# Kernel tuning notes

Measured on AMD Instinct MI355X. Metric: run time of the kernel, lower is better.

The kernel has to match this reference:

```python
import jax, jax.numpy as jnp
import numpy as np

INPUT_SIZE = 2
EMB = 64
RNN = 128
EDGE_RNN = 128
OUT = 5
N = 500000


def setup_inputs() -> dict:
    key = jax.random.key(0)
    ks = jax.random.split(key, 12)
    s = 0.1
    return {
        "pos": jax.random.normal(ks[0], (N, INPUT_SIZE), jnp.float32),
        "h_other": jax.random.normal(ks[1], (N, 2 * EDGE_RNN), jnp.float32),
        "h": jax.random.normal(ks[2], (N, RNN), jnp.float32),
        "enc_W": jax.random.normal(ks[3], (EMB, INPUT_SIZE), jnp.float32) * s,
        "enc_b": jnp.zeros((EMB,), jnp.float32),
        "henc_W": jax.random.normal(ks[4], (EMB, 2 * EDGE_RNN), jnp.float32) * s,
        "henc_b": jnp.zeros((EMB,), jnp.float32),
        "W_ih": jax.random.normal(ks[5], (3 * RNN, 2 * EMB), jnp.float32) * s,
        "b_ih": jax.random.normal(ks[6], (3 * RNN,), jnp.float32) * s,
        "W_hh": jax.random.normal(ks[7], (3 * RNN, RNN), jnp.float32) * s,
        "b_hh": jax.random.normal(ks[8], (3 * RNN,), jnp.float32) * s,
        "dec_W": jax.random.normal(ks[9], (OUT, RNN), jnp.float32) * s,
        "dec_b": jnp.zeros((OUT,), jnp.float32),
    }


def reference(pos, h_other, h, enc_W, enc_b, henc_W, henc_b,
              W_ih, b_ih, W_hh, b_hh, dec_W, dec_b):
    # encode position and edge-RNN hidden states
    enc_in = jax.nn.relu(pos @ enc_W.T + enc_b)          # [N, EMB]
    enc_hid = jax.nn.relu(h_other @ henc_W.T + henc_b)   # [N, EMB]
    x = jnp.concatenate([enc_in, enc_hid], axis=1)       # [N, 2*EMB]
    # GRUCell (torch gate order: reset, update, new)
    gx = x @ W_ih.T + b_ih                               # [N, 3*RNN]
    gh = h @ W_hh.T + b_hh                               # [N, 3*RNN]
    xr, xz, xn = jnp.split(gx, 3, axis=1)
    hr, hz, hn = jnp.split(gh, 3, axis=1)
    r = jax.nn.sigmoid(xr + hr)
    z = jax.nn.sigmoid(xz + hz)
    n = jnp.tanh(xn + r * hn)
    h_new = (1.0 - z) * n + z * h                        # [N, RNN]
    out = h_new @ dec_W.T + dec_b                        # [N, OUT]
    return (out, h_new)
```

## Files before the change

kernel.cpp:

```cpp
#include <hip/hip_runtime.h>
#include <hip/hip_bf16.h>
#include <stdint.h>

typedef __bf16 bf16x8 __attribute__((ext_vector_type(8)));
typedef float f32x4 __attribute__((ext_vector_type(4)));

#define WS_WIH 0
#define WS_WHH 49152
#define WS_HENC 98304
#define WS_DEC 114688
#define WS_TOTAL 116736

#define LDS_X  0
#define LDS_H  16384
#define LDS_SZ 32768

__device__ __forceinline__ unsigned short f2bf(float f) {
    unsigned u = __float_as_uint(f);
    unsigned r = (u + 0x7FFFu + ((u >> 16) & 1u)) >> 16;
    return (unsigned short)r;
}
__device__ __forceinline__ float bf2f(unsigned short u) {
    return __uint_as_float(((unsigned)u) << 16);
}

__device__ __forceinline__ unsigned cvt_pk_bf16(float a, float b) {
    unsigned r;
    asm("v_cvt_pk_bf16_f32 %0, %1, %2" : "=v"(r) : "v"(a), "v"(b));
    return r;
}

__device__ __forceinline__ float fast_rcp(float x) { return __builtin_amdgcn_rcpf(x); }
__device__ __forceinline__ float sigmf(float x) { return fast_rcp(1.0f + __expf(-x)); }
__device__ __forceinline__ float tanh_fast(float x) {
    float t = __expf(-2.0f * fabsf(x));
    float r = (1.0f - t) * fast_rcp(1.0f + t);
    return copysignf(r, x);
}

__global__ void convert_weights_kernel(const float* __restrict__ wih,
                                       const float* __restrict__ whh,
                                       const float* __restrict__ henc,
                                       const float* __restrict__ dec,
                                       unsigned short* __restrict__ ws) {
    int i = blockIdx.x * 256 + threadIdx.x;
    if (i >= WS_TOTAL) return;
    float v;
    if (i < WS_WHH)        v = wih[i];
    else if (i < WS_HENC)  v = whh[i - WS_WHH];
    else if (i < WS_DEC)   v = henc[i - WS_HENC];
    else { int d = i - WS_DEC; v = (d < 640) ? dec[d] : 0.0f; }
    ws[i] = f2bf(v);
}

__launch_bounds__(256, 2)
__global__ void fused_rnn_kernel(const float* __restrict__ pos,
                                 const float* __restrict__ h_other,
                                 const float* __restrict__ h,
                                 const float* __restrict__ enc_W,
                                 const float* __restrict__ enc_b,
                                 const float* __restrict__ henc_b,
                                 const float* __restrict__ b_ih,
                                 const float* __restrict__ b_hh,
                                 const float* __restrict__ dec_b,
                                 const unsigned short* __restrict__ ws,
                                 float* __restrict__ out,
                                 float* __restrict__ hnew,
                                 int N) {
    __shared__ char sm[LDS_SZ];
    const int tid = threadIdx.x;
    const int w   = tid >> 6;
    const int l   = tid & 63;
    const int lg  = l >> 4;
    const int ln  = l & 15;
    const int row0 = blockIdx.x * 64;

    #pragma unroll
    for (int j = 0; j < 8; ++j) {
        int e0  = (tid + 256 * j) * 4;
        int row = e0 >> 7;
        int col = e0 & 127;
        int grow = row0 + row; if (grow > N - 1) grow = N - 1;
        float4 v = *reinterpret_cast<const float4*>(h + (size_t)grow * 128 + col);
        uint2 p;
        p.x = cvt_pk_bf16(v.x, v.y);
        p.y = cvt_pk_bf16(v.z, v.w);
        int boff = LDS_H + row * 256 + ((col * 2) ^ ((row & 7) << 4));
        *reinterpret_cast<uint2*>(sm + boff) = p;
    }
    {
        int row = tid >> 2;
        int c0  = (tid & 3) * 16;
        int grow = row0 + row; if (grow > N - 1) grow = N - 1;
        float p0 = pos[(size_t)grow * 2 + 0];
        float p1 = pos[(size_t)grow * 2 + 1];
        #pragma unroll
        for (int q = 0; q < 8; ++q) {
            int c = c0 + q * 2;
            float v0 = fmaxf(p0 * enc_W[c * 2]     + p1 * enc_W[c * 2 + 1] + enc_b[c], 0.f);
            float v1 = fmaxf(p0 * enc_W[c * 2 + 2] + p1 * enc_W[c * 2 + 3] + enc_b[c + 1], 0.f);
            unsigned pk = cvt_pk_bf16(v0, v1);
            int boff = LDS_X + row * 256 + ((c * 2) ^ ((row & 7) << 4));
            *reinterpret_cast<unsigned*>(sm + boff) = pk;
        }
    }

    {
        bf16x8 Bh[8];
        const unsigned short* hb = ws + WS_HENC + (size_t)(16 * w + ln) * 256;
        #pragma unroll
        for (int ks = 0; ks < 8; ++ks)
            Bh[ks] = *reinterpret_cast<const bf16x8*>(hb + ks * 32 + lg * 8);

        f32x4 e2[4];
        #pragma unroll
        for (int mt = 0; mt < 4; ++mt) e2[mt] = (f32x4){0.f, 0.f, 0.f, 0.f};
        #pragma unroll
        for (int mt = 0; mt < 4; ++mt) {
            int grow = row0 + 16 * mt + ln; if (grow > N - 1) grow = N - 1;
            const float* rp = h_other + (size_t)grow * 256 + lg * 8;
            #pragma unroll
            for (int ks = 0; ks < 8; ++ks) {
                const float* ap = rp + ks * 32;
                float4 a0 = *reinterpret_cast<const float4*>(ap);
                float4 a1 = *reinterpret_cast<const float4*>(ap + 4);
                union { unsigned u[4]; bf16x8 b; } af;
                af.u[0] = cvt_pk_bf16(a0.x, a0.y);
                af.u[1] = cvt_pk_bf16(a0.z, a0.w);
                af.u[2] = cvt_pk_bf16(a1.x, a1.y);
                af.u[3] = cvt_pk_bf16(a1.z, a1.w);
                e2[mt] = __builtin_amdgcn_mfma_f32_16x16x32_bf16(af.b, Bh[ks], e2[mt], 0, 0, 0);
            }
        }
        int col = 16 * w + ln;
        float bias = henc_b[col];
        #pragma unroll
        for (int mt = 0; mt < 4; ++mt)
            #pragma unroll
            for (int i = 0; i < 4; ++i) {
                int row = 16 * mt + lg * 4 + i;
                float v = fmaxf(e2[mt][i] + bias, 0.f);
                *reinterpret_cast<unsigned short*>(
                    sm + LDS_X + row * 256 + (((64 + col) * 2) ^ ((row & 7) << 4))) = f2bf(v);
            }
    }
    __syncthreads();

    f32x4 acc[4][8];
    #pragma unroll
    for (int a = 0; a < 4; ++a)
        #pragma unroll
        for (int b = 0; b < 8; ++b) acc[a][b] = (f32x4){0.f, 0.f, 0.f, 0.f};

    const unsigned short* WIH = ws + WS_WIH;
    const unsigned short* WHH = ws + WS_WHH;

    #pragma unroll
    for (int t = 0; t < 8; ++t) {
        const int abase = (t < 4) ? LDS_X : LDS_H;
        const int kb = (t & 3) * 64;
        bf16x8 Af[4];
        #pragma unroll
        for (int mt = 0; mt < 4; ++mt) {
            int row = 16 * mt + ln;
            Af[mt] = *reinterpret_cast<const bf16x8*>(
                sm + abase + row * 256 + ((kb + lg * 16) ^ ((row & 7) << 4)));
        }
        const int kk = (t & 3) * 32 + lg * 8;

        #define MFMA_JOB(job, Wptr, ob) { \
            bf16x8 bfr = *reinterpret_cast<const bf16x8*>((Wptr) + (size_t)((ob) + ln) * 128 + kk); \
            acc[0][job] = __builtin_amdgcn_mfma_f32_16x16x32_bf16(Af[0], bfr, acc[0][job], 0, 0, 0); \
            acc[1][job] = __builtin_amdgcn_mfma_f32_16x16x32_bf16(Af[1], bfr, acc[1][job], 0, 0, 0); \
            acc[2][job] = __builtin_amdgcn_mfma_f32_16x16x32_bf16(Af[2], bfr, acc[2][job], 0, 0, 0); \
            acc[3][job] = __builtin_amdgcn_mfma_f32_16x16x32_bf16(Af[3], bfr, acc[3][job], 0, 0, 0); }

        if (t < 4) {
            MFMA_JOB(0, WIH, 32 * w);
            MFMA_JOB(1, WIH, 32 * w + 16);
            MFMA_JOB(2, WIH, 128 + 32 * w);
            MFMA_JOB(3, WIH, 144 + 32 * w);
            MFMA_JOB(4, WIH, 256 + 32 * w);
            MFMA_JOB(5, WIH, 272 + 32 * w);
        } else {
            MFMA_JOB(0, WHH, 32 * w);
            MFMA_JOB(1, WHH, 32 * w + 16);
            MFMA_JOB(2, WHH, 128 + 32 * w);
            MFMA_JOB(3, WHH, 144 + 32 * w);
            MFMA_JOB(6, WHH, 256 + 32 * w);
            MFMA_JOB(7, WHH, 272 + 32 * w);
        }
        #undef MFMA_JOB
    }

    __syncthreads();

    #pragma unroll
    for (int jt = 0; jt < 2; ++jt) {
        int j = 32 * w + 16 * jt + ln;
        float br  = b_ih[j] + b_hh[j];
        float bz  = b_ih[128 + j] + b_hh[128 + j];
        float bxn = b_ih[256 + j];
        float bhn = b_hh[256 + j];
        #pragma unroll
        for (int mt = 0; mt < 4; ++mt)
            #pragma unroll
            for (int i = 0; i < 4; ++i) {
                int row = mt * 16 + lg * 4 + i;
                int grow = row0 + row;
                float r  = sigmf(acc[mt][jt][i] + br);
                float z  = sigmf(acc[mt][2 + jt][i] + bz);
                float xn = acc[mt][4 + jt][i] + bxn;
                float hn = acc[mt][6 + jt][i] + bhn;
                float nn = tanh_fast(xn + r * hn);
                unsigned short hu = *reinterpret_cast<const unsigned short*>(
                    sm + LDS_H + row * 256 + ((j * 2) ^ ((row & 7) << 4)));
                float hp = bf2f(hu);
                float hv = (1.0f - z) * nn + z * hp;
                if (grow < N) hnew[(size_t)grow * 128 + j] = hv;
                *reinterpret_cast<unsigned short*>(
                    sm + LDS_X + row * 256 + ((j * 2) ^ ((row & 7) << 4))) = f2bf(hv);
            }
    }
    __syncthreads();

    {
        f32x4 oc = (f32x4){0.f, 0.f, 0.f, 0.f};
        #pragma unroll
        for (int ks = 0; ks < 4; ++ks) {
            int row = 16 * w + ln;
            bf16x8 af = *reinterpret_cast<const bf16x8*>(
                sm + LDS_X + row * 256 + ((ks * 64 + lg * 16) ^ ((row & 7) << 4)));
            bf16x8 bf = *reinterpret_cast<const bf16x8*>(ws + WS_DEC + ln * 128 + ks * 32 + lg * 8);
            oc = __builtin_amdgcn_mfma_f32_16x16x32_bf16(af, bf, oc, 0, 0, 0);
        }
        if (ln < 5) {
            float bias = dec_b[ln];
            #pragma unroll
            for (int i = 0; i < 4; ++i) {
                int grow = row0 + 16 * w + lg * 4 + i;
                if (grow < N) out[(size_t)grow * 5 + ln] = oc[i] + bias;
            }
        }
    }
}

extern "C" void kernel_launch(void* const* d_in, const int* in_sizes, int n_in,
                              void* d_out, int out_size, void* d_ws, size_t ws_size,
                              hipStream_t stream) {
    const float* pos     = (const float*)d_in[0];
    const float* h_other = (const float*)d_in[1];
    const float* h       = (const float*)d_in[2];
    const float* enc_W   = (const float*)d_in[3];
    const float* enc_b   = (const float*)d_in[4];
    const float* henc_W  = (const float*)d_in[5];
    const float* henc_b  = (const float*)d_in[6];
    const float* W_ih    = (const float*)d_in[7];
    const float* b_ih    = (const float*)d_in[8];
    const float* W_hh    = (const float*)d_in[9];
    const float* b_hh    = (const float*)d_in[10];
    const float* dec_W   = (const float*)d_in[11];
    const float* dec_b   = (const float*)d_in[12];

    int N = in_sizes[0] / 2;
    unsigned short* ws = (unsigned short*)d_ws;
    float* out  = (float*)d_out;
    float* hnew = out + (size_t)N * 5;

    hipLaunchKernelGGL(convert_weights_kernel, dim3((WS_TOTAL + 255) / 256), dim3(256), 0, stream,
                       W_ih, W_hh, henc_W, dec_W, ws);
    int blocks = (N + 63) / 64;
    hipLaunchKernelGGL(fused_rnn_kernel, dim3(blocks), dim3(256), 0, stream,
                       pos, h_other, h, enc_W, enc_b, henc_b, b_ih, b_hh, dec_b,
                       ws, out, hnew, N);
}
```

Baseline: 556.3 us.

## Use 512-thread blocks with per-wave gate columns and double-buffered weight fragments

Doubles the workgroup to 8 waves per 64-row tile, so each wave owns 16 hidden columns and computes all three gates for them, with half the accumulators. Weight fragments are software-pipelined with ping-pong registers so the next k-step's global loads are issued before the current MFMAs. The h_other encoder loads are batched before conversion, and the henc and decoder weights are hoisted. The aim is more latency hiding and less register pressure per wave. In exchange each wave issues fewer MFMAs, and half the waves sit idle in the decoder stage.

```diff
diff --git a/kernel.cpp b/kernel.cpp
--- a/kernel.cpp
+++ b/kernel.cpp
@@ -53,7 +53,7 @@
     ws[i] = f2bf(v);
 }
 
-__launch_bounds__(256, 2)
+__launch_bounds__(512, 2)
 __global__ void fused_rnn_kernel(const float* __restrict__ pos,
                                  const float* __restrict__ h_other,
                                  const float* __restrict__ h,
@@ -75,9 +75,18 @@
     const int ln  = l & 15;
     const int row0 = blockIdx.x * 64;
 
+    const int nt = w & 3;
+    bf16x8 Bh[8];
+    {
+        const unsigned short* hb = ws + WS_HENC + (size_t)(16 * nt + ln) * 256;
+        #pragma unroll
+        for (int ks = 0; ks < 8; ++ks)
+            Bh[ks] = *reinterpret_cast<const bf16x8*>(hb + ks * 32 + lg * 8);
+    }
+
     #pragma unroll
-    for (int j = 0; j < 8; ++j) {
-        int e0  = (tid + 256 * j) * 4;
+    for (int j = 0; j < 4; ++j) {
+        int e0  = (tid + 512 * j) * 4;
         int row = e0 >> 7;
         int col = e0 & 127;
         int grow = row0 + row; if (grow > N - 1) grow = N - 1;
@@ -89,13 +98,13 @@
         *reinterpret_cast<uint2*>(sm + boff) = p;
     }
     {
-        int row = tid >> 2;
-        int c0  = (tid & 3) * 16;
+        int row = tid >> 3;
+        int c0  = (tid & 7) * 8;
         int grow = row0 + row; if (grow > N - 1) grow = N - 1;
         float p0 = pos[(size_t)grow * 2 + 0];
         float p1 = pos[(size_t)grow * 2 + 1];
         #pragma unroll
-        for (int q = 0; q < 8; ++q) {
+        for (int q = 0; q < 4; ++q) {
             int c = c0 + q * 2;
             float v0 = fmaxf(p0 * enc_W[c * 2]     + p1 * enc_W[c * 2 + 1] + enc_b[c], 0.f);
             float v1 = fmaxf(p0 * enc_W[c * 2 + 2] + p1 * enc_W[c * 2 + 3] + enc_b[c + 1], 0.f);
@@ -106,133 +115,138 @@
     }
 
     {
-        bf16x8 Bh[8];
-        const unsigned short* hb = ws + WS_HENC + (size_t)(16 * w + ln) * 256;
-        #pragma unroll
-        for (int ks = 0; ks < 8; ++ks)
-            Bh[ks] = *reinterpret_cast<const bf16x8*>(hb + ks * 32 + lg * 8);
-
-        f32x4 e2[4];
-        #pragma unroll
-        for (int mt = 0; mt < 4; ++mt) e2[mt] = (f32x4){0.f, 0.f, 0.f, 0.f};
-        #pragma unroll
-        for (int mt = 0; mt < 4; ++mt) {
+        f32x4 e2[2];
+        #pragma unroll
+        for (int m2 = 0; m2 < 2; ++m2) e2[m2] = (f32x4){0.f, 0.f, 0.f, 0.f};
+        #pragma unroll
+        for (int m2 = 0; m2 < 2; ++m2) {
+            int mt = (w >> 2) * 2 + m2;
             int grow = row0 + 16 * mt + ln; if (grow > N - 1) grow = N - 1;
             const float* rp = h_other + (size_t)grow * 256 + lg * 8;
+            float4 hb0[8], hb1[8];
             #pragma unroll
             for (int ks = 0; ks < 8; ++ks) {
-                const float* ap = rp + ks * 32;
-                float4 a0 = *reinterpret_cast<const float4*>(ap);
-                float4 a1 = *reinterpret_cast<const float4*>(ap + 4);
+                hb0[ks] = *reinterpret_cast<const float4*>(rp + ks * 32);
+                hb1[ks] = *reinterpret_cast<const float4*>(rp + ks * 32 + 4);
+            }
+            #pragma unroll
+            for (int ks = 0; ks < 8; ++ks) {
                 union { unsigned u[4]; bf16x8 b; } af;
-                af.u[0] = cvt_pk_bf16(a0.x, a0.y);
-                af.u[1] = cvt_pk_bf16(a0.z, a0.w);
-                af.u[2] = cvt_pk_bf16(a1.x, a1.y);
-                af.u[3] = cvt_pk_bf16(a1.z, a1.w);
-                e2[mt] = __builtin_amdgcn_mfma_f32_16x16x32_bf16(af.b, Bh[ks], e2[mt], 0, 0, 0);
-            }
-        }
-        int col = 16 * w + ln;
+                af.u[0] = cvt_pk_bf16(hb0[ks].x, hb0[ks].y);
+                af.u[1] = cvt_pk_bf16(hb0[ks].z, hb0[ks].w);
+                af.u[2] = cvt_pk_bf16(hb1[ks].x, hb1[ks].y);
+                af.u[3] = cvt_pk_bf16(hb1[ks].z, hb1[ks].w);
+                e2[m2] = __builtin_amdgcn_mfma_f32_16x16x32_bf16(af.b, Bh[ks], e2[m2], 0, 0, 0);
+            }
+        }
+        int col = 16 * nt + ln;
         float bias = henc_b[col];
         #pragma unroll
-        for (int mt = 0; mt < 4; ++mt)
+        for (int m2 = 0; m2 < 2; ++m2) {
+            int mt = (w >> 2) * 2 + m2;
             #pragma unroll
             for (int i = 0; i < 4; ++i) {
                 int row = 16 * mt + lg * 4 + i;
-                float v = fmaxf(e2[mt][i] + bias, 0.f);
+                float v = fmaxf(e2[m2][i] + bias, 0.f);
                 *reinterpret_cast<unsigned short*>(
                     sm + LDS_X + row * 256 + (((64 + col) * 2) ^ ((row & 7) << 4))) = f2bf(v);
             }
-    }
+        }
+    }
+
+    const unsigned short* WIH = ws + WS_WIH;
+    const unsigned short* WHH = ws + WS_WHH;
+    const int jrow = 16 * w + ln;
+
+    #define LOADW(d0, d1, d2, Wp, kk) { \
+        d0 = *reinterpret_cast<const bf16x8*>((Wp) + (size_t)(jrow) * 128 + (kk)); \
+        d1 = *reinterpret_cast<const bf16x8*>((Wp) + (size_t)(128 + jrow) * 128 + (kk)); \
+        d2 = *reinterpret_cast<const bf16x8*>((Wp) + (size_t)(256 + jrow) * 128 + (kk)); }
+
+    bf16x8 Ba0, Ba1, Ba2, Bb0, Bb1, Bb2;
+    LOADW(Ba0, Ba1, Ba2, WIH, lg * 8);
+    float br  = b_ih[jrow] + b_hh[jrow];
+    float bz  = b_ih[128 + jrow] + b_hh[128 + jrow];
+    float bxn = b_ih[256 + jrow];
+    float bhn = b_hh[256 + jrow];
+
     __syncthreads();
 
-    f32x4 acc[4][8];
+    f32x4 acc[4][4];
     #pragma unroll
     for (int a = 0; a < 4; ++a)
         #pragma unroll
-        for (int b = 0; b < 8; ++b) acc[a][b] = (f32x4){0.f, 0.f, 0.f, 0.f};
-
-    const unsigned short* WIH = ws + WS_WIH;
-    const unsigned short* WHH = ws + WS_WHH;
+        for (int b = 0; b < 4; ++b) acc[a][b] = (f32x4){0.f, 0.f, 0.f, 0.f};
+
+    #define GSTEP(t, C0, C1, C2, N0, N1, N2) { \
+        if ((t) < 7) { \
+            const unsigned short* Wp = (((t) + 1) < 4) ? WIH : WHH; \
+            const int kkn = ((((t) + 1) & 3) * 32) + lg * 8; \
+            LOADW(N0, N1, N2, Wp, kkn); \
+        } \
+        const int abase = ((t) < 4) ? LDS_X : LDS_H; \
+        const int kb = ((t) & 3) * 64; \
+        bf16x8 Af[4]; \
+        _Pragma("unroll") \
+        for (int mt = 0; mt < 4; ++mt) { \
+            int row = 16 * mt + ln; \
+            Af[mt] = *reinterpret_cast<const bf16x8*>( \
+                sm + abase + row * 256 + ((kb + lg * 16) ^ ((row & 7) << 4))); \
+        } \
+        const int nj = ((t) < 4) ? 2 : 3; \
+        _Pragma("unroll") \
+        for (int mt = 0; mt < 4; ++mt) { \
+            acc[mt][0]  = __builtin_amdgcn_mfma_f32_16x16x32_bf16(Af[mt], C0, acc[mt][0], 0, 0, 0); \
+            acc[mt][1]  = __builtin_amdgcn_mfma_f32_16x16x32_bf16(Af[mt], C1, acc[mt][1], 0, 0, 0); \
+            acc[mt][nj] = __builtin_amdgcn_mfma_f32_16x16x32_bf16(Af[mt], C2, acc[mt][nj], 0, 0, 0); \
+        } }
+
+    GSTEP(0, Ba0, Ba1, Ba2, Bb0, Bb1, Bb2);
+    GSTEP(1, Bb0, Bb1, Bb2, Ba0, Ba1, Ba2);
+    GSTEP(2, Ba0, Ba1, Ba2, Bb0, Bb1, Bb2);
+    GSTEP(3, Bb0, Bb1, Bb2, Ba0, Ba1, Ba2);
+    GSTEP(4, Ba0, Ba1, Ba2, Bb0, Bb1, Bb2);
+    GSTEP(5, Bb0, Bb1, Bb2, Ba0, Ba1, Ba2);
+    GSTEP(6, Ba0, Ba1, Ba2, Bb0, Bb1, Bb2);
+    GSTEP(7, Bb0, Bb1, Bb2, Ba0, Ba1, Ba2);
+    #undef GSTEP
+    #undef LOADW
+
+    __syncthreads();
 
     #pragma unroll
-    for (int t = 0; t < 8; ++t) {
-        const int abase = (t < 4) ? LDS_X : LDS_H;
-        const int kb = (t & 3) * 64;
-        bf16x8 Af[4];
-        #pragma unroll
-        for (int mt = 0; mt < 4; ++mt) {
-            int row = 16 * mt + ln;
-            Af[mt] = *reinterpret_cast<const bf16x8*>(
-                sm + abase + row * 256 + ((kb + lg * 16) ^ ((row & 7) << 4)));
-        }
-        const int kk = (t & 3) * 32 + lg * 8;
-
-        #define MFMA_JOB(job, Wptr, ob) { \
-            bf16x8 bfr = *reinterpret_cast<const bf16x8*>((Wptr) + (size_t)((ob) + ln) * 128 + kk); \
-            acc[0][job] = __builtin_amdgcn_mfma_f32_16x16x32_bf16(Af[0], bfr, acc[0][job], 0, 0, 0); \
-            acc[1][job] = __builtin_amdgcn_mfma_f32_16x16x32_bf16(Af[1], bfr, acc[1][job], 0, 0, 0); \
-            acc[2][job] = __builtin_amdgcn_mfma_f32_16x16x32_bf16(Af[2], bfr, acc[2][job], 0, 0, 0); \
-            acc[3][job] = __builtin_amdgcn_mfma_f32_16x16x32_bf16(Af[3], bfr, acc[3][job], 0, 0, 0); }
-
-        if (t < 4) {
-            MFMA_JOB(0, WIH, 32 * w);
-            MFMA_JOB(1, WIH, 32 * w + 16);
-            MFMA_JOB(2, WIH, 128 + 32 * w);
-            MFMA_JOB(3, WIH, 144 + 32 * w);
-            MFMA_JOB(4, WIH, 256 + 32 * w);
-            MFMA_JOB(5, WIH, 272 + 32 * w);
-        } else {
-            MFMA_JOB(0, WHH, 32 * w);
-            MFMA_JOB(1, WHH, 32 * w + 16);
-            MFMA_JOB(2, WHH, 128 + 32 * w);
-            MFMA_JOB(3, WHH, 144 + 32 * w);
-            MFMA_JOB(6, WHH, 256 + 32 * w);
-            MFMA_JOB(7, WHH, 272 + 32 * w);
-        }
-        #undef MFMA_JOB
-    }
-
+    for (int mt = 0; mt < 4; ++mt)
+        #pragma unroll
+        for (int i = 0; i < 4; ++i) {
+            int row = mt * 16 + lg * 4 + i;
+            int grow = row0 + row;
+            float r  = sigmf(acc[mt][0][i] + br);
+            float z  = sigmf(acc[mt][1][i] + bz);
+            float xn = acc[mt][2][i] + bxn;
+            float hn = acc[mt][3][i] + bhn;
+            float nn = tanh_fast(xn + r * hn);
+            unsigned short hu = *reinterpret_cast<const unsigned short*>(
+                sm + LDS_H + row * 256 + ((jrow * 2) ^ ((row & 7) << 4)));
+            float hp = bf2f(hu);
+            float hv = (1.0f - z) * nn + z * hp;
+            if (grow < N) hnew[(size_t)grow * 128 + jrow] = hv;
+            *reinterpret_cast<unsigned short*>(
+                sm + LDS_X + row * 256 + ((jrow * 2) ^ ((row & 7) << 4))) = f2bf(hv);
+        }
     __syncthreads();
 
-    #pragma unroll
-    for (int jt = 0; jt < 2; ++jt) {
-        int j = 32 * w + 16 * jt + ln;
-        float br  = b_ih[j] + b_hh[j];
-        float bz  = b_ih[128 + j] + b_hh[128 + j];
-        float bxn = b_ih[256 + j];
-        float bhn = b_hh[256 + j];
-        #pragma unroll
-        for (int mt = 0; mt < 4; ++mt)
-            #pragma unroll
-            for (int i = 0; i < 4; ++i) {
-                int row = mt * 16 + lg * 4 + i;
-                int grow = row0 + row;
-                float r  = sigmf(acc[mt][jt][i] + br);
-                float z  = sigmf(acc[mt][2 + jt][i] + bz);
-                float xn = acc[mt][4 + jt][i] + bxn;
-                float hn = acc[mt][6 + jt][i] + bhn;
-                float nn = tanh_fast(xn + r * hn);
-                unsigned short hu = *reinterpret_cast<const unsigned short*>(
-                    sm + LDS_H + row * 256 + ((j * 2) ^ ((row & 7) << 4)));
-                float hp = bf2f(hu);
-                float hv = (1.0f - z) * nn + z * hp;
-                if (grow < N) hnew[(size_t)grow * 128 + j] = hv;
-                *reinterpret_cast<unsigned short*>(
-                    sm + LDS_X + row * 256 + ((j * 2) ^ ((row & 7) << 4))) = f2bf(hv);
-            }
-    }
-    __syncthreads();
-
-    {
+    if (w < 4) {
+        bf16x8 dbf[4];
+        #pragma unroll
+        for (int ks = 0; ks < 4; ++ks)
+            dbf[ks] = *reinterpret_cast<const bf16x8*>(ws + WS_DEC + ln * 128 + ks * 32 + lg * 8);
         f32x4 oc = (f32x4){0.f, 0.f, 0.f, 0.f};
         #pragma unroll
         for (int ks = 0; ks < 4; ++ks) {
             int row = 16 * w + ln;
             bf16x8 af = *reinterpret_cast<const bf16x8*>(
                 sm + LDS_X + row * 256 + ((ks * 64 + lg * 16) ^ ((row & 7) << 4)));
-            bf16x8 bf = *reinterpret_cast<const bf16x8*>(ws + WS_DEC + ln * 128 + ks * 32 + lg * 8);
-            oc = __builtin_amdgcn_mfma_f32_16x16x32_bf16(af, bf, oc, 0, 0, 0);
+            oc = __builtin_amdgcn_mfma_f32_16x16x32_bf16(af, dbf[ks], oc, 0, 0, 0);
         }
         if (ln < 5) {
             float bias = dec_b[ln];
@@ -270,7 +284,7 @@
     hipLaunchKernelGGL(convert_weights_kernel, dim3((WS_TOTAL + 255) / 256), dim3(256), 0, stream,
                        W_ih, W_hh, henc_W, dec_W, ws);
     int blocks = (N + 63) / 64;
-    hipLaunchKernelGGL(fused_rnn_kernel, dim3(blocks), dim3(256), 0, stream,
+    hipLaunchKernelGGL(fused_rnn_kernel, dim3(blocks), dim3(512), 0, stream,
                        pos, h_other, h, enc_W, enc_b, henc_b, b_ih, b_hh, dec_b,
                        ws, out, hnew, N);
 }
```

New measurement: 590.3 us. +6.1%, slower.
